# Optimization experiments

Hardware: AMD Instinct MI355X
Metric: run time of the kernel (lower is better)

Reference implementation:

```python
import jax, jax.numpy as jnp
import numpy as np

B, L, D, H, NL, F, C = 32, 512, 512, 8, 6, 2048, 9
HD = D // H
SCALE = float(np.sqrt(HD))
EPS = 1e-5


def _layernorm(x, g, b):
    mu = jnp.mean(x, axis=-1, keepdims=True)
    var = jnp.mean((x - mu) ** 2, axis=-1, keepdims=True)
    return (x - mu) * jax.lax.rsqrt(var + EPS) * g + b


def setup_inputs() -> dict:
    key = jax.random.key(0)
    ks = jax.random.split(key, 16)
    s = 0.02
    return {
        "x": jax.random.normal(ks[0], (B, L, D), jnp.float32),
        "case_ids": jax.random.randint(ks[1], (B, L), 0, C),
        "attention_mask": jnp.ones((B, L), jnp.int32),
        "Wq": jax.random.normal(ks[2], (NL, D, D), jnp.float32) * s,
        "bq": jnp.zeros((NL, D), jnp.float32),
        "Wk": jax.random.normal(ks[3], (NL, D, D), jnp.float32) * s,
        "bk": jnp.zeros((NL, D), jnp.float32),
        "Wv": jax.random.normal(ks[4], (NL, D, D), jnp.float32) * s,
        "bv": jnp.zeros((NL, D), jnp.float32),
        "Wo": jax.random.normal(ks[5], (NL, D, D), jnp.float32) * s,
        "bo": jnp.zeros((NL, D), jnp.float32),
        "ln1_g": jnp.ones((NL, D), jnp.float32),
        "ln1_b": jnp.zeros((NL, D), jnp.float32),
        "ln2_g": jnp.ones((NL, D), jnp.float32),
        "ln2_b": jnp.zeros((NL, D), jnp.float32),
        "W1": jax.random.normal(ks[6], (NL, D, F), jnp.float32) * s,
        "b1": jnp.zeros((NL, F), jnp.float32),
        "W2": jax.random.normal(ks[7], (NL, F, D), jnp.float32) * s,
        "b2": jnp.zeros((NL, D), jnp.float32),
        "case_bias": jax.random.normal(ks[8], (NL, H, C, C), jnp.float32) * 0.1,
        "verb_bias": jax.random.normal(ks[9], (NL, H), jnp.float32) * 0.1,
        "fn_g": jnp.ones((D,), jnp.float32),
        "fn_b": jnp.zeros((D,), jnp.float32),
    }


def reference(x, case_ids, attention_mask, Wq, bq, Wk, bk, Wv, bv, Wo, bo,
              ln1_g, ln1_b, ln2_g, ln2_b, W1, b1, W2, b2,
              case_bias, verb_bias, fn_g, fn_b):
    dt = x.dtype
    # causal + padding additive mask: [B, 1, L, L]
    causal = jnp.triu(jnp.full((L, L), -10000.0, dtype=dt), k=1)[None, None]
    pad = (1.0 - attention_mask.astype(dt))[:, None, None, :] * -10000.0
    mask = causal + pad
    verb_mask = (case_ids == 8).astype(dt)  # [B, L]
    ci, cj = case_ids[:, :, None], case_ids[:, None, :]  # [B,L,1], [B,1,L]

    for i in range(NL):
        h = _layernorm(x, ln1_g[i], ln1_b[i])
        q = (h @ Wq[i] + bq[i]).reshape(B, L, H, HD).transpose(0, 2, 1, 3)
        k = (h @ Wk[i] + bk[i]).reshape(B, L, H, HD).transpose(0, 2, 1, 3)
        v = (h @ Wv[i] + bv[i]).reshape(B, L, H, HD).transpose(0, 2, 1, 3)
        scores = jnp.einsum('bhqd,bhkd->bhqk', q, k) / SCALE
        # Panini grammatical bias: per-head pairwise case bias + verb key bias
        pbias = case_bias[i][:, ci, cj]  # [H, B, L, L]
        scores = scores + jnp.transpose(pbias, (1, 0, 2, 3))
        scores = scores + verb_bias[i][None, :, None, None] * verb_mask[:, None, None, :]
        scores = scores + mask
        w = jax.nn.softmax(scores, axis=-1)
        attn = jnp.einsum('bhqk,bhkd->bhqd', w, v).transpose(0, 2, 1, 3).reshape(B, L, D)
        x = x + attn @ Wo[i] + bo[i]
        h2 = _layernorm(x, ln2_g[i], ln2_b[i])
        ff = jax.nn.gelu(h2 @ W1[i] + b1[i], approximate=False) @ W2[i] + b2[i]
        x = x + ff
    return _layernorm(x, fn_g, fn_b)
```

## Files before the change

### kernel.cpp

```cpp
#include <hip/hip_runtime.h>
#include <hip/hip_bf16.h>

#define B_   32
#define L_   512
#define D_   512
#define H_   8
#define NL_  6
#define F_   2048
#define C_   9
#define HD_  64
#define MTOK 16384

typedef __bf16 bf16x8 __attribute__((ext_vector_type(8)));
typedef __bf16 bf16x4 __attribute__((ext_vector_type(4)));
typedef float  f32x4  __attribute__((ext_vector_type(4)));

#define MFMA16(a,b,c) __builtin_amdgcn_mfma_f32_16x16x32_bf16((a),(b),(c),0,0,0)
#define GLD16(g,l) __builtin_amdgcn_global_load_lds( \
    (const __attribute__((address_space(1))) void*)(g), \
    (__attribute__((address_space(3))) void*)(l), 16, 0, 0)

__global__ __launch_bounds__(256) void transpose_w(
    const float* __restrict__ in, __hip_bfloat16* __restrict__ out,
    int K, int N, size_t zso)
{
    __shared__ float t[32][33];
    const int z = blockIdx.z;
    const float* src = in + (size_t)z * K * N;
    __hip_bfloat16* dst = out + (size_t)z * zso;
    const int n0 = blockIdx.x * 32, k0 = blockIdx.y * 32;
    const int tx = threadIdx.x, ty = threadIdx.y;
#pragma unroll
    for (int r = ty; r < 32; r += 8)
        t[r][tx] = src[(size_t)(k0 + r) * N + n0 + tx];
    __syncthreads();
#pragma unroll
    for (int r = ty; r < 32; r += 8)
        dst[(size_t)(n0 + r) * K + k0 + tx] = __float2bfloat16(t[tx][r]);
}

__global__ void copy_f32x4(const float4* __restrict__ in, float4* __restrict__ out, int n)
{
    int i = blockIdx.x * blockDim.x + threadIdx.x;
    if (i < n) out[i] = in[i];
}

template <typename OUT>
__global__ __launch_bounds__(256) void ln_kernel(
    const float* __restrict__ x, const float* __restrict__ g,
    const float* __restrict__ be, OUT* __restrict__ out)
{
    const int row  = blockIdx.x * 4 + (threadIdx.x >> 6);
    const int lane = threadIdx.x & 63;
    const int c0   = lane * 8;
    const float* xr = x + (size_t)row * D_ + c0;
    float4 a = *(const float4*)xr;
    float4 c = *(const float4*)(xr + 4);
    float v[8] = {a.x, a.y, a.z, a.w, c.x, c.y, c.z, c.w};

    float s = 0.f;
#pragma unroll
    for (int j = 0; j < 8; ++j) s += v[j];
#pragma unroll
    for (int o = 1; o < 64; o <<= 1) s += __shfl_xor(s, o, 64);
    const float mu = s * (1.0f / D_);

    float s2 = 0.f;
#pragma unroll
    for (int j = 0; j < 8; ++j) { float d = v[j] - mu; s2 += d * d; }
#pragma unroll
    for (int o = 1; o < 64; o <<= 1) s2 += __shfl_xor(s2, o, 64);
    const float rs = rsqrtf(s2 * (1.0f / D_) + 1e-5f);

    float4 g0 = *(const float4*)(g + c0);
    float4 g1 = *(const float4*)(g + c0 + 4);
    float4 b0 = *(const float4*)(be + c0);
    float4 b1 = *(const float4*)(be + c0 + 4);
    float gg[8] = {g0.x, g0.y, g0.z, g0.w, g1.x, g1.y, g1.z, g1.w};
    float bb[8] = {b0.x, b0.y, b0.z, b0.w, b1.x, b1.y, b1.z, b1.w};

    if constexpr (sizeof(OUT) == 2) {
        bf16x8 o8;
#pragma unroll
        for (int j = 0; j < 8; ++j)
            o8[j] = (__bf16)((v[j] - mu) * rs * gg[j] + bb[j]);
        *(bf16x8*)((__hip_bfloat16*)out + (size_t)row * D_ + c0) = o8;
    } else {
        float* op = (float*)out + (size_t)row * D_ + c0;
        float4 r0, r1;
        r0.x = (v[0]-mu)*rs*gg[0]+bb[0]; r0.y = (v[1]-mu)*rs*gg[1]+bb[1];
        r0.z = (v[2]-mu)*rs*gg[2]+bb[2]; r0.w = (v[3]-mu)*rs*gg[3]+bb[3];
        r1.x = (v[4]-mu)*rs*gg[4]+bb[4]; r1.y = (v[5]-mu)*rs*gg[5]+bb[5];
        r1.z = (v[6]-mu)*rs*gg[6]+bb[6]; r1.w = (v[7]-mu)*rs*gg[7]+bb[7];
        *(float4*)op = r0; *(float4*)(op + 4) = r1;
    }
}

__device__ __forceinline__ float gelu_tanh(float v)
{
    const float t2 = v * v;
    const float u  = v * (0.7978845608028654f + 0.0356774081363001f * t2);
    const float a  = __builtin_fabsf(u);
    const float e  = __expf(-2.0f * a);
    const float r  = __builtin_amdgcn_rcpf(1.0f + e);
    const float th = (1.0f - e) * r;
    return 0.5f * v + 0.5f * __builtin_fabsf(v) * th;
}

template <int EPI, int WM>
__global__ __launch_bounds__(WM * 128, (WM == 4) ? 4 : 3) void gemm_r5(
    const __hip_bfloat16* __restrict__ A,
    const __hip_bfloat16* __restrict__ BT,
    const float* __restrict__ bias0, const float* __restrict__ bias1,
    const float* __restrict__ bias2,
    void* __restrict__ out0, void* __restrict__ out1, void* __restrict__ out2,
    const float* __restrict__ Res, int Ndim, int K)
{
    constexpr int THREADS = WM * 128;
    constexpr int BM = WM * 64;
    __shared__ __align__(16) __hip_bfloat16 As[3][BM * 32];
    __shared__ __align__(16) __hip_bfloat16 Bs[3][128 * 32];

    const int tid = threadIdx.x;
    const int w = tid >> 6, lane = tid & 63;
    const int lq = lane & 15, lg = lane >> 4;
    const int wm = w >> 1, wn = w & 1;
    const int RB = wm * 64, CB = wn * 64;

    const int gX = gridDim.x;
    const int nwg = gX * gridDim.y;
    int flat = blockIdx.y * gX + blockIdx.x;
    {
        const int qq = nwg >> 3, rr = nwg & 7;
        const int xcd = flat & 7, off = flat >> 3;
        flat = (xcd < rr ? xcd * (qq + 1) : rr * (qq + 1) + (xcd - rr) * qq) + off;
    }
    const int bx = flat % gX, by = flat / gX;
    const int m0 = by * BM, n0 = bx * 128;

    const int rc = tid >> 2;
    const int sc = ((tid & 3) ^ ((rc >> 1) & 3)) * 8;
    const __hip_bfloat16* gA0 = A  + (size_t)(m0 + rc) * K + sc;
    const __hip_bfloat16* gB0 = BT + (size_t)(n0 + rc) * K + sc;

    auto STAGE = [&](int tt) {
        const size_t ko = (size_t)tt * 32;
        const int sl = tt % 3;
        char* ab = (char*)As[sl] + w * 1024;
        GLD16(gA0 + ko, ab);
        GLD16(gA0 + (size_t)(THREADS / 4) * K + ko, ab + THREADS * 16);
        char* bb = (char*)Bs[sl] + w * 1024;
        GLD16(gB0 + ko, bb);
        if constexpr (WM == 2)
            GLD16(gB0 + (size_t)64 * K + ko, bb + 4096);
    };

    const int rsw = (lq >> 1) & 3;
    const int aoff = (RB + lq) * 64 + ((lg ^ rsw) << 4);
    const int boff = (CB + lq) * 64 + ((lg ^ rsw) << 4);

    f32x4 acc[4][4] = {};
    const int NTt = K >> 5;

    STAGE(0); STAGE(1);

    for (int t = 0; t < NTt; ++t) {
        if (t + 1 < NTt) {
            if constexpr (WM == 4) asm volatile("s_waitcnt vmcnt(3)" ::: "memory");
            else                   asm volatile("s_waitcnt vmcnt(4)" ::: "memory");
        } else {
            asm volatile("s_waitcnt vmcnt(0)" ::: "memory");
        }
        __builtin_amdgcn_s_barrier();
        __builtin_amdgcn_sched_barrier(0);

        const char* ca = (const char*)As[t % 3];
        const char* cb = (const char*)Bs[t % 3];
        bf16x8 af[4], bf[4];
#pragma unroll
        for (int fm = 0; fm < 4; ++fm) af[fm] = *(const bf16x8*)(ca + aoff + fm * 1024);
#pragma unroll
        for (int fn = 0; fn < 4; ++fn) bf[fn] = *(const bf16x8*)(cb + boff + fn * 1024);

        if (t + 2 < NTt) STAGE(t + 2);

        __builtin_amdgcn_s_setprio(1);
#pragma unroll
        for (int fm = 0; fm < 4; ++fm)
#pragma unroll
            for (int fn = 0; fn < 4; ++fn)
                acc[fm][fn] = MFMA16(af[fm], bf[fn], acc[fm][fn]);
        __builtin_amdgcn_s_setprio(0);
    }

    if constexpr (EPI == 4) {
        const int sec = n0 >> 9;
        const int nb = (n0 & 511) + CB;
        const float* bp = sec == 0 ? bias0 : (sec == 1 ? bias1 : bias2);
        float bcol[4];
#pragma unroll
        for (int fn = 0; fn < 4; ++fn) bcol[fn] = bp[nb + fn * 16 + lq];
        if (sec < 2) {
            __hip_bfloat16* op = (__hip_bfloat16*)(sec == 0 ? out0 : out1);
#pragma unroll
            for (int fm = 0; fm < 4; ++fm)
#pragma unroll
                for (int fn = 0; fn < 4; ++fn)
#pragma unroll
                    for (int r = 0; r < 4; ++r) {
                        const int m = m0 + RB + fm * 16 + lg * 4 + r;
                        op[(size_t)m * 512 + nb + fn * 16 + lq] =
                            __float2bfloat16(acc[fm][fn][r] + bcol[fn]);
                    }
        } else {
            __hip_bfloat16* vp = (__hip_bfloat16*)out2;
            const int bb = m0 >> 9;
            const int l0 = (m0 & 511) + RB + lg * 4;
#pragma unroll
            for (int fm = 0; fm < 4; ++fm)
#pragma unroll
                for (int fn = 0; fn < 4; ++fn) {
                    bf16x4 pv;
#pragma unroll
                    for (int r = 0; r < 4; ++r)
                        pv[r] = (__bf16)(acc[fm][fn][r] + bcol[fn]);
                    *(bf16x4*)(vp + ((size_t)(bb * 512 + nb + fn * 16 + lq)) * 512
                               + l0 + fm * 16) = pv;
                }
        }
    } else {
        float bcol[4];
#pragma unroll
        for (int fn = 0; fn < 4; ++fn) bcol[fn] = bias0[n0 + CB + fn * 16 + lq];
#pragma unroll
        for (int fm = 0; fm < 4; ++fm)
#pragma unroll
            for (int fn = 0; fn < 4; ++fn) {
                const int n = n0 + CB + fn * 16 + lq;
#pragma unroll
                for (int r = 0; r < 4; ++r) {
                    const int m = m0 + RB + fm * 16 + lg * 4 + r;
                    float v = acc[fm][fn][r] + bcol[fn];
                    if constexpr (EPI == 1) {
                        float* Co = (float*)out0;
                        const size_t idx = (size_t)m * Ndim + n;
                        Co[idx] = Res[idx] + v;
                    } else {
                        ((__hip_bfloat16*)out0)[(size_t)m * Ndim + n] =
                            __float2bfloat16(gelu_tanh(v));
                    }
                }
            }
    }
}

__global__ __launch_bounds__(256) void attn_kernel(
    const __hip_bfloat16* __restrict__ Q, const __hip_bfloat16* __restrict__ K,
    const __hip_bfloat16* __restrict__ VT, __hip_bfloat16* __restrict__ Out,
    const int* __restrict__ case_ids, const int* __restrict__ amask,
    const float* __restrict__ case_bias, const float* __restrict__ verb_bias,
    int layer)
{
    __shared__ __align__(16) __bf16 Ks[2][64 * 64];
    __shared__ __align__(16) __bf16 Vs[2][64 * 64];
    __shared__ __align__(16) __bf16 Pl[4][16 * 64];
    __shared__ __bf16 Bia[9][520];

    const int bh = blockIdx.x;
    const int b = bh >> 3, hh = bh & 7;
    const int qc = blockIdx.y;
    const int t = threadIdx.x;
    const int w = t >> 6, lane = t & 63;
    const int lq = lane & 15, lg = lane >> 4;
    const int swz = lq & 7;

    const int rA = w * 16 + (lane >> 3);
    const int swsrc = ((lane & 7) ^ (lane >> 3)) << 4;
    const __hip_bfloat16* kg0 = K  + ((size_t)b * L_ + rA) * D_ + hh * HD_;
    const __hip_bfloat16* vg0 = VT + ((size_t)b * D_ + hh * HD_ + rA) * L_;

    auto stage = [&](int buf, int kv0) {
        const char* gk = (const char*)(kg0 + (size_t)kv0 * D_) + swsrc;
        GLD16(gk,                      (char*)Ks[buf] + w * 2048);
        GLD16(gk + (size_t)8 * D_ * 2, (char*)Ks[buf] + w * 2048 + 1024);
        const char* gv = (const char*)(vg0 + kv0) + swsrc;
        GLD16(gv,                      (char*)Vs[buf] + w * 2048);
        GLD16(gv + (size_t)8 * L_ * 2, (char*)Vs[buf] + w * 2048 + 1024);
    };

    const float vb = verb_bias[layer * H_ + hh];
    const float* cb = case_bias + ((size_t)layer * H_ + hh) * (C_ * C_);
    for (int idx = t; idx < 9 * 512; idx += 256) {
        const int ci = idx >> 9, kv = idx & 511;
        const int cj = case_ids[b * L_ + kv];
        Bia[ci][kv] = (__bf16)(cb[ci * C_ + cj] + (cj == 8 ? vb : 0.f)
                               - 10000.f * (1.f - (float)amask[b * L_ + kv]));
    }
    __syncthreads();

    stage(0, 0);

    const int qloc = w * 16 + lq;
    const int qrow = qc * 64 + qloc;
    const int ci_q = case_ids[b * L_ + qrow];
    const __hip_bfloat16* qp = Q + ((size_t)b * L_ + qrow) * D_ + hh * HD_;
    const bf16x8 qf0 = *(const bf16x8*)(qp + lg * 8);
    const bf16x8 qf1 = *(const bf16x8*)(qp + 32 + lg * 8);

    float m_run = -1e30f, l_run = 0.f;
    f32x4 o[4] = {};
    const int ntiles = qc + 1;
    int cur = 0;

    for (int kt = 0; kt < ntiles; ++kt) {
        if (kt) __builtin_amdgcn_s_barrier();
        if (kt + 1 < ntiles) {
            stage(cur ^ 1, (kt + 1) * 64);
            asm volatile("s_waitcnt vmcnt(4)" ::: "memory");
        } else {
            asm volatile("s_waitcnt vmcnt(0)" ::: "memory");
        }
        __builtin_amdgcn_s_barrier();
        __builtin_amdgcn_sched_barrier(0);

        const char* kb  = (const char*)Ks[cur];
        const char* vb2 = (const char*)Vs[cur];

        f32x4 s[4] = {};
        __builtin_amdgcn_s_setprio(1);
#pragma unroll
        for (int c = 0; c < 4; ++c) {
            const bf16x8 ka = *(const bf16x8*)(kb + (16 * c + lq) * 128 + ((lg ^ swz) << 4));
            s[c] = MFMA16(ka, qf0, s[c]);
            const bf16x8 kc = *(const bf16x8*)(kb + (16 * c + lq) * 128 + (((4 + lg) ^ swz) << 4));
            s[c] = MFMA16(kc, qf1, s[c]);
        }
        __builtin_amdgcn_s_setprio(0);

        const __bf16* brow = &Bia[ci_q][kt * 64];
        const bool dtile = (kt == qc);
        float xs[16];
#pragma unroll
        for (int c = 0; c < 4; ++c) {
            const bf16x4 bb = *(const bf16x4*)(brow + 16 * c + lg * 4);
#pragma unroll
            for (int r = 0; r < 4; ++r) {
                const int kvl = 16 * c + lg * 4 + r;
                float v = s[c][r] * 0.125f + (float)bb[r];
                xs[4 * c + r] = (dtile && (kvl > qloc)) ? -1e9f : v;
            }
        }

        float a0 = fmaxf(fmaxf(xs[0], xs[1]),  fmaxf(xs[2], xs[3]));
        float a1 = fmaxf(fmaxf(xs[4], xs[5]),  fmaxf(xs[6], xs[7]));
        float a2 = fmaxf(fmaxf(xs[8], xs[9]),  fmaxf(xs[10], xs[11]));
        float a3 = fmaxf(fmaxf(xs[12], xs[13]), fmaxf(xs[14], xs[15]));
        float pmax = fmaxf(fmaxf(a0, a1), fmaxf(a2, a3));
        pmax = fmaxf(pmax, __shfl_xor(pmax, 16, 64));
        pmax = fmaxf(pmax, __shfl_xor(pmax, 32, 64));

        const float mnew = fmaxf(m_run, pmax);
        const float corr = __expf(m_run - mnew);
        float p[16], ps0 = 0.f, ps1 = 0.f;
#pragma unroll
        for (int j = 0; j < 16; j += 2) {
            p[j]     = __expf(xs[j] - mnew);     ps0 += p[j];
            p[j + 1] = __expf(xs[j + 1] - mnew); ps1 += p[j + 1];
        }
        float ps = ps0 + ps1;
        ps += __shfl_xor(ps, 16, 64);
        ps += __shfl_xor(ps, 32, 64);
        l_run = l_run * corr + ps;
        m_run = mnew;

        float cr[4];
#pragma unroll
        for (int r = 0; r < 4; ++r) cr[r] = __shfl(corr, lg * 4 + r, 64);
#pragma unroll
        for (int nt = 0; nt < 4; ++nt)
#pragma unroll
            for (int r = 0; r < 4; ++r) o[nt][r] *= cr[r];

        char* pw = (char*)Pl[w];
#pragma unroll
        for (int c = 0; c < 4; ++c) {
            bf16x4 pv;
#pragma unroll
            for (int r = 0; r < 4; ++r) pv[r] = (__bf16)p[4 * c + r];
            const int slot = (2 * c + (lg >> 1)) ^ swz;
            *(bf16x4*)(pw + lq * 128 + (slot << 4) + ((lg & 1) << 3)) = pv;
        }

        __builtin_amdgcn_s_setprio(1);
#pragma unroll
        for (int hf = 0; hf < 2; ++hf) {
            const bf16x8 pf = *(const bf16x8*)(pw + lq * 128 + (((hf * 4 + lg) ^ swz) << 4));
#pragma unroll
            for (int nt = 0; nt < 4; ++nt) {
                const bf16x8 vf = *(const bf16x8*)(vb2 + (nt * 16 + lq) * 128
                                                   + (((hf * 4 + lg) ^ swz) << 4));
                o[nt] = MFMA16(pf, vf, o[nt]);
            }
        }
        __builtin_amdgcn_s_setprio(0);

        cur ^= 1;
    }

    const float inv = 1.f / l_run;
    float ir[4];
#pragma unroll
    for (int r = 0; r < 4; ++r) ir[r] = __shfl(inv, lg * 4 + r, 64);
    __hip_bfloat16* op = Out + ((size_t)b * L_ + qc * 64 + w * 16) * D_ + hh * HD_;
#pragma unroll
    for (int nt = 0; nt < 4; ++nt)
#pragma unroll
        for (int r = 0; r < 4; ++r)
            op[(size_t)(lg * 4 + r) * D_ + nt * 16 + lq] = __float2bfloat16(o[nt][r] * ir[r]);
}

extern "C" void kernel_launch(void* const* d_in, const int* in_sizes, int n_in,
                              void* d_out, int out_size, void* d_ws, size_t ws_size,
                              hipStream_t stream)
{
    const float* x_in  = (const float*)d_in[0];
    const int*   cids  = (const int*)  d_in[1];
    const int*   amask = (const int*)  d_in[2];
    const float* Wq = (const float*)d_in[3];
    const float* bq = (const float*)d_in[4];
    const float* Wk = (const float*)d_in[5];
    const float* bk = (const float*)d_in[6];
    const float* Wv = (const float*)d_in[7];
    const float* bv = (const float*)d_in[8];
    const float* Wo = (const float*)d_in[9];
    const float* bo = (const float*)d_in[10];
    const float* ln1g = (const float*)d_in[11];
    const float* ln1b = (const float*)d_in[12];
    const float* ln2g = (const float*)d_in[13];
    const float* ln2b = (const float*)d_in[14];
    const float* W1 = (const float*)d_in[15];
    const float* b1 = (const float*)d_in[16];
    const float* W2 = (const float*)d_in[17];
    const float* b2 = (const float*)d_in[18];
    const float* cbias = (const float*)d_in[19];
    const float* vbias = (const float*)d_in[20];
    const float* fng = (const float*)d_in[21];
    const float* fnb = (const float*)d_in[22];

    char* w = (char*)d_ws;
    float* x_ws = (float*)w;                 w += (size_t)MTOK * D_ * 4;
    __hip_bfloat16* hbuf = (__hip_bfloat16*)w; w += (size_t)MTOK * D_ * 2;
    __hip_bfloat16* qbuf = (__hip_bfloat16*)w; w += (size_t)MTOK * D_ * 2;
    __hip_bfloat16* kbuf = (__hip_bfloat16*)w; w += (size_t)MTOK * D_ * 2;
    __hip_bfloat16* vtb  = (__hip_bfloat16*)w; w += (size_t)MTOK * D_ * 2;
    __hip_bfloat16* ffb  = (__hip_bfloat16*)w; w += (size_t)MTOK * F_ * 2;
    __hip_bfloat16* WqkvT = (__hip_bfloat16*)w; w += (size_t)NL_ * 3 * D_ * D_ * 2;
    __hip_bfloat16* WoT  = (__hip_bfloat16*)w; w += (size_t)NL_ * D_ * D_ * 2;
    __hip_bfloat16* W1T  = (__hip_bfloat16*)w; w += (size_t)NL_ * D_ * F_ * 2;
    __hip_bfloat16* W2T  = (__hip_bfloat16*)w; w += (size_t)NL_ * D_ * F_ * 2;

    const size_t qkvZ = (size_t)3 * D_ * D_;
    const dim3 tb(32, 8);
    transpose_w<<<dim3(D_/32, D_/32, NL_), tb, 0, stream>>>(Wq, WqkvT,           D_, D_, qkvZ);
    transpose_w<<<dim3(D_/32, D_/32, NL_), tb, 0, stream>>>(Wk, WqkvT + D_*D_,   D_, D_, qkvZ);
    transpose_w<<<dim3(D_/32, D_/32, NL_), tb, 0, stream>>>(Wv, WqkvT + 2*D_*D_, D_, D_, qkvZ);
    transpose_w<<<dim3(D_/32, D_/32, NL_), tb, 0, stream>>>(Wo, WoT, D_, D_, (size_t)D_*D_);
    transpose_w<<<dim3(F_/32, D_/32, NL_), tb, 0, stream>>>(W1, W1T, D_, F_, (size_t)D_*F_);
    transpose_w<<<dim3(D_/32, F_/32, NL_), tb, 0, stream>>>(W2, W2T, F_, D_, (size_t)D_*F_);

    copy_f32x4<<<8192, 256, 0, stream>>>((const float4*)x_in, (float4*)x_ws,
                                         MTOK * D_ / 4);

    const dim3 gQKV(12, 64);
    const dim3 gO(4, 128);
    const dim3 gW1(16, 64);
    const dim3 gW2(4, 128);

    for (int i = 0; i < NL_; ++i) {
        ln_kernel<__hip_bfloat16><<<MTOK/4, 256, 0, stream>>>(
            x_ws, ln1g + i * D_, ln1b + i * D_, hbuf);

        gemm_r5<4, 4><<<gQKV, 512, 0, stream>>>(hbuf, WqkvT + (size_t)i * qkvZ,
            bq + i*D_, bk + i*D_, bv + i*D_, qbuf, kbuf, vtb, nullptr, 512, D_);

        attn_kernel<<<dim3(B_ * H_, L_/64), 256, 0, stream>>>(
            qbuf, kbuf, vtb, hbuf, cids, amask, cbias, vbias, i);

        gemm_r5<1, 2><<<gO, 256, 0, stream>>>(hbuf, WoT + (size_t)i*D_*D_,
            bo + i*D_, nullptr, nullptr, x_ws, nullptr, nullptr, x_ws, D_, D_);

        ln_kernel<__hip_bfloat16><<<MTOK/4, 256, 0, stream>>>(
            x_ws, ln2g + i * D_, ln2b + i * D_, hbuf);

        gemm_r5<2, 4><<<gW1, 512, 0, stream>>>(hbuf, W1T + (size_t)i*D_*F_,
            b1 + i*F_, nullptr, nullptr, ffb, nullptr, nullptr, nullptr, F_, D_);

        gemm_r5<1, 2><<<gW2, 256, 0, stream>>>(ffb, W2T + (size_t)i*D_*F_,
            b2 + i*D_, nullptr, nullptr, x_ws, nullptr, nullptr, x_ws, D_, F_);
    }

    ln_kernel<float><<<MTOK/4, 256, 0, stream>>>(x_ws, fng, fnb, (float*)d_out);
}
```

Before: 1.326 ms.

## Pair causal query chunks per block and precompute attention bias table globally

The attention kernel now handles two query chunks per block (chunk i and 7-i), so every block does the same amount of causal work and the K/V tiles it loads are shared by both chunks. The per-block shared-memory bias build is replaced by a one-time global bf16 bias table covering all layers, batches, heads and case ids, which the kernel reads directly. The QKV GEMM also moves to a smaller tile configuration with more blocks. In exchange the kernel holds more live registers, capped by the launch bound of 4, and needs extra workspace plus a prologue pass to build the table.

After: 1.277 ms. -3.6%, faster.

```diff
diff --git a/kernel.cpp b/kernel.cpp
--- a/kernel.cpp
+++ b/kernel.cpp
@@ -43,6 +43,24 @@
 {
     int i = blockIdx.x * blockDim.x + threadIdx.x;
     if (i < n) out[i] = in[i];
+}
+
+__global__ __launch_bounds__(256) void bias_build(
+    const int* __restrict__ case_ids, const int* __restrict__ amask,
+    const float* __restrict__ cbias, const float* __restrict__ vbias,
+    __hip_bfloat16* __restrict__ tab)
+{
+    const unsigned idx = blockIdx.x * 256 + threadIdx.x;
+    const int kv = idx & 511;
+    unsigned r = idx >> 9;
+    const int ci = r % 9; r /= 9;
+    const int hh = r % H_; r /= H_;
+    const int b = r % B_; const int l = r / B_;
+    const int cj = case_ids[b * L_ + kv];
+    const float v = cbias[(((size_t)l * H_ + hh) * C_ + ci) * C_ + cj]
+                  + (cj == 8 ? vbias[l * H_ + hh] : 0.f)
+                  - 10000.f * (1.f - (float)amask[b * L_ + kv]);
+    tab[idx] = __float2bfloat16(v);
 }
 
 template <typename OUT>
@@ -254,21 +272,20 @@
     }
 }
 
-__global__ __launch_bounds__(256) void attn_kernel(
+__global__ __launch_bounds__(256, 4) void attn_kernel(
     const __hip_bfloat16* __restrict__ Q, const __hip_bfloat16* __restrict__ K,
     const __hip_bfloat16* __restrict__ VT, __hip_bfloat16* __restrict__ Out,
-    const int* __restrict__ case_ids, const int* __restrict__ amask,
-    const float* __restrict__ case_bias, const float* __restrict__ verb_bias,
+    const int* __restrict__ case_ids, const __hip_bfloat16* __restrict__ tab,
     int layer)
 {
     __shared__ __align__(16) __bf16 Ks[2][64 * 64];
     __shared__ __align__(16) __bf16 Vs[2][64 * 64];
     __shared__ __align__(16) __bf16 Pl[4][16 * 64];
-    __shared__ __bf16 Bia[9][520];
 
     const int bh = blockIdx.x;
     const int b = bh >> 3, hh = bh & 7;
-    const int qc = blockIdx.y;
+    const int qcA = blockIdx.y;
+    const int qcB = 7 - qcA;
     const int t = threadIdx.x;
     const int w = t >> 6, lane = t & 63;
     const int lq = lane & 15, lg = lane >> 4;
@@ -288,33 +305,110 @@
         GLD16(gv + (size_t)8 * L_ * 2, (char*)Vs[buf] + w * 2048 + 1024);
     };
 
-    const float vb = verb_bias[layer * H_ + hh];
-    const float* cb = case_bias + ((size_t)layer * H_ + hh) * (C_ * C_);
-    for (int idx = t; idx < 9 * 512; idx += 256) {
-        const int ci = idx >> 9, kv = idx & 511;
-        const int cj = case_ids[b * L_ + kv];
-        Bia[ci][kv] = (__bf16)(cb[ci * C_ + cj] + (cj == 8 ? vb : 0.f)
-                               - 10000.f * (1.f - (float)amask[b * L_ + kv]));
-    }
-    __syncthreads();
-
     stage(0, 0);
 
     const int qloc = w * 16 + lq;
-    const int qrow = qc * 64 + qloc;
-    const int ci_q = case_ids[b * L_ + qrow];
-    const __hip_bfloat16* qp = Q + ((size_t)b * L_ + qrow) * D_ + hh * HD_;
-    const bf16x8 qf0 = *(const bf16x8*)(qp + lg * 8);
-    const bf16x8 qf1 = *(const bf16x8*)(qp + 32 + lg * 8);
-
-    float m_run = -1e30f, l_run = 0.f;
-    f32x4 o[4] = {};
-    const int ntiles = qc + 1;
+    const int qrowA = qcA * 64 + qloc;
+    const int qrowB = qcB * 64 + qloc;
+    const size_t tbase = (((size_t)layer * B_ + b) * H_ + hh) * C_;
+    const __hip_bfloat16* ciqA = tab + (tbase + case_ids[b * L_ + qrowA]) * L_;
+    const __hip_bfloat16* ciqB = tab + (tbase + case_ids[b * L_ + qrowB]) * L_;
+
+    const __hip_bfloat16* qpA = Q + ((size_t)b * L_ + qrowA) * D_ + hh * HD_;
+    const __hip_bfloat16* qpB = Q + ((size_t)b * L_ + qrowB) * D_ + hh * HD_;
+    const bf16x8 qfA0 = *(const bf16x8*)(qpA + lg * 8);
+    const bf16x8 qfA1 = *(const bf16x8*)(qpA + 32 + lg * 8);
+    const bf16x8 qfB0 = *(const bf16x8*)(qpB + lg * 8);
+    const bf16x8 qfB1 = *(const bf16x8*)(qpB + 32 + lg * 8);
+
+    float mA = -1e30f, lA = 0.f, mB = -1e30f, lB = 0.f;
+    f32x4 oA[4] = {}, oB[4] = {};
     int cur = 0;
 
-    for (int kt = 0; kt < ntiles; ++kt) {
+    auto process = [&](const bf16x8 qf0, const bf16x8 qf1,
+                       const __hip_bfloat16* ciq, int qcX,
+                       float& m_run, float& l_run, f32x4* o,
+                       const char* kb, const char* vb2, int kt) {
+        bf16x4 bb[4];
+#pragma unroll
+        for (int c = 0; c < 4; ++c)
+            bb[c] = *(const bf16x4*)(ciq + kt * 64 + 16 * c + lg * 4);
+
+        f32x4 s[4] = {};
+        __builtin_amdgcn_s_setprio(1);
+#pragma unroll
+        for (int c = 0; c < 4; ++c) {
+            const bf16x8 ka = *(const bf16x8*)(kb + (16 * c + lq) * 128 + ((lg ^ swz) << 4));
+            s[c] = MFMA16(ka, qf0, s[c]);
+            const bf16x8 kc = *(const bf16x8*)(kb + (16 * c + lq) * 128 + (((4 + lg) ^ swz) << 4));
+            s[c] = MFMA16(kc, qf1, s[c]);
+        }
+        __builtin_amdgcn_s_setprio(0);
+
+        const bool dtile = (kt == qcX);
+        float xs[16];
+#pragma unroll
+        for (int c = 0; c < 4; ++c)
+#pragma unroll
+            for (int r = 0; r < 4; ++r) {
+                const int kvl = 16 * c + lg * 4 + r;
+                float v = s[c][r] * 0.125f + (float)bb[c][r];
+                xs[4 * c + r] = (dtile && (kvl > qloc)) ? -1e9f : v;
+            }
+
+        float a0 = fmaxf(fmaxf(xs[0], xs[1]),  fmaxf(xs[2], xs[3]));
+        float a1 = fmaxf(fmaxf(xs[4], xs[5]),  fmaxf(xs[6], xs[7]));
+        float a2 = fmaxf(fmaxf(xs[8], xs[9]),  fmaxf(xs[10], xs[11]));
+        float a3 = fmaxf(fmaxf(xs[12], xs[13]), fmaxf(xs[14], xs[15]));
+        float pmax = fmaxf(fmaxf(a0, a1), fmaxf(a2, a3));
+        pmax = fmaxf(pmax, __shfl_xor(pmax, 16, 64));
+        pmax = fmaxf(pmax, __shfl_xor(pmax, 32, 64));
+
+        const float mnew = fmaxf(m_run, pmax);
+        const float corr = __expf(m_run - mnew);
+        float ps = 0.f;
+#pragma unroll
+        for (int j = 0; j < 16; ++j) { xs[j] = __expf(xs[j] - mnew); ps += xs[j]; }
+        ps += __shfl_xor(ps, 16, 64);
+        ps += __shfl_xor(ps, 32, 64);
+        l_run = l_run * corr + ps;
+        m_run = mnew;
+
+        float cr[4];
+#pragma unroll
+        for (int r = 0; r < 4; ++r) cr[r] = __shfl(corr, lg * 4 + r, 64);
+#pragma unroll
+        for (int nt = 0; nt < 4; ++nt)
+#pragma unroll
+            for (int r = 0; r < 4; ++r) o[nt][r] *= cr[r];
+
+        char* pw = (char*)Pl[w];
+#pragma unroll
+        for (int c = 0; c < 4; ++c) {
+            bf16x4 pv;
+#pragma unroll
+            for (int r = 0; r < 4; ++r) pv[r] = (__bf16)xs[4 * c + r];
+            const int slot = (2 * c + (lg >> 1)) ^ swz;
+            *(bf16x4*)(pw + lq * 128 + (slot << 4) + ((lg & 1) << 3)) = pv;
+        }
+
+        __builtin_amdgcn_s_setprio(1);
+#pragma unroll
+        for (int hf = 0; hf < 2; ++hf) {
+            const bf16x8 pf = *(const bf16x8*)(pw + lq * 128 + (((hf * 4 + lg) ^ swz) << 4));
+#pragma unroll
+            for (int nt = 0; nt < 4; ++nt) {
+                const bf16x8 vf = *(const bf16x8*)(vb2 + (nt * 16 + lq) * 128
+                                                   + (((hf * 4 + lg) ^ swz) << 4));
+                o[nt] = MFMA16(pf, vf, o[nt]);
+            }
+        }
+        __builtin_amdgcn_s_setprio(0);
+    };
+
+    for (int kt = 0; kt <= qcB; ++kt) {
         if (kt) __builtin_amdgcn_s_barrier();
-        if (kt + 1 < ntiles) {
+        if (kt < qcB) {
             stage(cur ^ 1, (kt + 1) * 64);
             asm volatile("s_waitcnt vmcnt(4)" ::: "memory");
         } else {
@@ -326,97 +420,27 @@
         const char* kb  = (const char*)Ks[cur];
         const char* vb2 = (const char*)Vs[cur];
 
-        f32x4 s[4] = {};
-        __builtin_amdgcn_s_setprio(1);
-#pragma unroll
-        for (int c = 0; c < 4; ++c) {
-            const bf16x8 ka = *(const bf16x8*)(kb + (16 * c + lq) * 128 + ((lg ^ swz) << 4));
-            s[c] = MFMA16(ka, qf0, s[c]);
-            const bf16x8 kc = *(const bf16x8*)(kb + (16 * c + lq) * 128 + (((4 + lg) ^ swz) << 4));
-            s[c] = MFMA16(kc, qf1, s[c]);
-        }
-        __builtin_amdgcn_s_setprio(0);
-
-        const __bf16* brow = &Bia[ci_q][kt * 64];
-        const bool dtile = (kt == qc);
-        float xs[16];
-#pragma unroll
-        for (int c = 0; c < 4; ++c) {
-            const bf16x4 bb = *(const bf16x4*)(brow + 16 * c + lg * 4);
-#pragma unroll
-            for (int r = 0; r < 4; ++r) {
-                const int kvl = 16 * c + lg * 4 + r;
-                float v = s[c][r] * 0.125f + (float)bb[r];
-                xs[4 * c + r] = (dtile && (kvl > qloc)) ? -1e9f : v;
-            }
-        }
-
-        float a0 = fmaxf(fmaxf(xs[0], xs[1]),  fmaxf(xs[2], xs[3]));
-        float a1 = fmaxf(fmaxf(xs[4], xs[5]),  fmaxf(xs[6], xs[7]));
-        float a2 = fmaxf(fmaxf(xs[8], xs[9]),  fmaxf(xs[10], xs[11]));
-        float a3 = fmaxf(fmaxf(xs[12], xs[13]), fmaxf(xs[14], xs[15]));
-        float pmax = fmaxf(fmaxf(a0, a1), fmaxf(a2, a3));
-        pmax = fmaxf(pmax, __shfl_xor(pmax, 16, 64));
-        pmax = fmaxf(pmax, __shfl_xor(pmax, 32, 64));
-
-        const float mnew = fmaxf(m_run, pmax);
-        const float corr = __expf(m_run - mnew);
-        float p[16], ps0 = 0.f, ps1 = 0.f;
-#pragma unroll
-        for (int j = 0; j < 16; j += 2) {
-            p[j]     = __expf(xs[j] - mnew);     ps0 += p[j];
-            p[j + 1] = __expf(xs[j + 1] - mnew); ps1 += p[j + 1];
-        }
-        float ps = ps0 + ps1;
-        ps += __shfl_xor(ps, 16, 64);
-        ps += __shfl_xor(ps, 32, 64);
-        l_run = l_run * corr + ps;
-        m_run = mnew;
-
-        float cr[4];
-#pragma unroll
-        for (int r = 0; r < 4; ++r) cr[r] = __shfl(corr, lg * 4 + r, 64);
-#pragma unroll
-        for (int nt = 0; nt < 4; ++nt)
-#pragma unroll
-            for (int r = 0; r < 4; ++r) o[nt][r] *= cr[r];
-
-        char* pw = (char*)Pl[w];
-#pragma unroll
-        for (int c = 0; c < 4; ++c) {
-            bf16x4 pv;
-#pragma unroll
-            for (int r = 0; r < 4; ++r) pv[r] = (__bf16)p[4 * c + r];
-            const int slot = (2 * c + (lg >> 1)) ^ swz;
-            *(bf16x4*)(pw + lq * 128 + (slot << 4) + ((lg & 1) << 3)) = pv;
-        }
-
-        __builtin_amdgcn_s_setprio(1);
-#pragma unroll
-        for (int hf = 0; hf < 2; ++hf) {
-            const bf16x8 pf = *(const bf16x8*)(pw + lq * 128 + (((hf * 4 + lg) ^ swz) << 4));
-#pragma unroll
-            for (int nt = 0; nt < 4; ++nt) {
-                const bf16x8 vf = *(const bf16x8*)(vb2 + (nt * 16 + lq) * 128
-                                                   + (((hf * 4 + lg) ^ swz) << 4));
-                o[nt] = MFMA16(pf, vf, o[nt]);
-            }
-        }
-        __builtin_amdgcn_s_setprio(0);
-
+        process(qfB0, qfB1, ciqB, qcB, mB, lB, oB, kb, vb2, kt);
+        if (kt <= qcA)
+            process(qfA0, qfA1, ciqA, qcA, mA, lA, oA, kb, vb2, kt);
         cur ^= 1;
     }
 
-    const float inv = 1.f / l_run;
-    float ir[4];
-#pragma unroll
-    for (int r = 0; r < 4; ++r) ir[r] = __shfl(inv, lg * 4 + r, 64);
-    __hip_bfloat16* op = Out + ((size_t)b * L_ + qc * 64 + w * 16) * D_ + hh * HD_;
-#pragma unroll
-    for (int nt = 0; nt < 4; ++nt)
-#pragma unroll
-        for (int r = 0; r < 4; ++r)
-            op[(size_t)(lg * 4 + r) * D_ + nt * 16 + lq] = __float2bfloat16(o[nt][r] * ir[r]);
+    auto writeout = [&](float l_run, f32x4* o, int qcX) {
+        const float inv = 1.f / l_run;
+        float ir[4];
+#pragma unroll
+        for (int r = 0; r < 4; ++r) ir[r] = __shfl(inv, lg * 4 + r, 64);
+        __hip_bfloat16* op = Out + ((size_t)b * L_ + qcX * 64 + w * 16) * D_ + hh * HD_;
+#pragma unroll
+        for (int nt = 0; nt < 4; ++nt)
+#pragma unroll
+            for (int r = 0; r < 4; ++r)
+                op[(size_t)(lg * 4 + r) * D_ + nt * 16 + lq] =
+                    __float2bfloat16(o[nt][r] * ir[r]);
+    };
+    writeout(lA, oA, qcA);
+    writeout(lB, oB, qcB);
 }
 
 extern "C" void kernel_launch(void* const* d_in, const int* in_sizes, int n_in,
@@ -458,6 +482,7 @@
     __hip_bfloat16* WoT  = (__hip_bfloat16*)w; w += (size_t)NL_ * D_ * D_ * 2;
     __hip_bfloat16* W1T  = (__hip_bfloat16*)w; w += (size_t)NL_ * D_ * F_ * 2;
     __hip_bfloat16* W2T  = (__hip_bfloat16*)w; w += (size_t)NL_ * D_ * F_ * 2;
+    __hip_bfloat16* btab = (__hip_bfloat16*)w; w += (size_t)NL_ * B_ * H_ * C_ * L_ * 2;
 
     const size_t qkvZ = (size_t)3 * D_ * D_;
     const dim3 tb(32, 8);
@@ -468,10 +493,13 @@
     transpose_w<<<dim3(F_/32, D_/32, NL_), tb, 0, stream>>>(W1, W1T, D_, F_, (size_t)D_*F_);
     transpose_w<<<dim3(D_/32, F_/32, NL_), tb, 0, stream>>>(W2, W2T, F_, D_, (size_t)D_*F_);
 
+    bias_build<<<(NL_ * B_ * H_ * C_ * L_) / 256, 256, 0, stream>>>(
+        cids, amask, cbias, vbias, btab);
+
     copy_f32x4<<<8192, 256, 0, stream>>>((const float4*)x_in, (float4*)x_ws,
                                          MTOK * D_ / 4);
 
-    const dim3 gQKV(12, 64);
+    const dim3 gQKV(12, 128);
     const dim3 gO(4, 128);
     const dim3 gW1(16, 64);
     const dim3 gW2(4, 128);
@@ -480,11 +508,11 @@
         ln_kernel<__hip_bfloat16><<<MTOK/4, 256, 0, stream>>>(
             x_ws, ln1g + i * D_, ln1b + i * D_, hbuf);
 
-        gemm_r5<4, 4><<<gQKV, 512, 0, stream>>>(hbuf, WqkvT + (size_t)i * qkvZ,
+        gemm_r5<4, 2><<<gQKV, 256, 0, stream>>>(hbuf, WqkvT + (size_t)i * qkvZ,
             bq + i*D_, bk + i*D_, bv + i*D_, qbuf, kbuf, vtb, nullptr, 512, D_);
 
-        attn_kernel<<<dim3(B_ * H_, L_/64), 256, 0, stream>>>(
-            qbuf, kbuf, vtb, hbuf, cids, amask, cbias, vbias, i);
+        attn_kernel<<<dim3(B_ * H_, 4), 256, 0, stream>>>(
+            qbuf, kbuf, vtb, hbuf, cids, btab, i);
 
         gemm_r5<1, 2><<<gO, 256, 0, stream>>>(hbuf, WoT + (size_t)i*D_*D_,
             bo + i*D_, nullptr, nullptr, x_ws, nullptr, nullptr, x_ws, D_, D_);
```
